# Kernel tuning notes

Hardware: AMD Instinct MI355X
Metric: run time of the kernel (lower is better)

The kernel has to match this reference:

```python
import jax, jax.numpy as jnp
import numpy as np

N, C_DEC, H, W = 16, 512, 32, 32
C_ENC, S, FEATS_IN, N_HEAD = 768, 77, 512, 8
EPS = 1e-5


def setup_inputs() -> dict:
    key = jax.random.key(0)
    ks = jax.random.split(key, 12)
    inp = {
        "input": jax.random.normal(ks[0], (N, C_DEC, H, W), jnp.float32),
        "cond": jax.random.normal(ks[1], (N, FEATS_IN), jnp.float32),
        "enc_hidden": jax.random.normal(ks[2], (N, S, C_ENC), jnp.float32),
        "enc_padding_mask": jax.random.randint(ks[3], (N, S), 0, 2).astype(jnp.float32),
        # AdaGN linear: feats_in -> 2*c_dec (scales, shifts)
        "adagn_w": jax.random.normal(ks[4], (2 * C_DEC, FEATS_IN), jnp.float32) * 0.02,
        "adagn_b": jnp.zeros((2 * C_DEC,), jnp.float32),
        # LayerNorm(c_enc) affine
        "ln_w": jnp.ones((C_ENC,), jnp.float32),
        "ln_b": jnp.zeros((C_ENC,), jnp.float32),
        # 1x1 conv q projection (treated as channel matmul)
        "q_w": jax.random.normal(ks[5], (C_DEC, C_DEC), jnp.float32) * 0.02,
        "q_b": jnp.zeros((C_DEC,), jnp.float32),
        # kv linear: c_enc -> 2*c_dec
        "kv_w": jax.random.normal(ks[6], (2 * C_DEC, C_ENC), jnp.float32) * 0.02,
        "kv_b": jnp.zeros((2 * C_DEC,), jnp.float32),
        # 1x1 conv out projection
        "out_w": jax.random.normal(ks[7], (C_DEC, C_DEC), jnp.float32) * 0.02,
        "out_b": jnp.zeros((C_DEC,), jnp.float32),
    }
    return inp


def reference(input, cond, enc_hidden, enc_padding_mask,
              adagn_w, adagn_b, ln_w, ln_b,
              q_w, q_b, kv_w, kv_b, out_w, out_b):
    n, c, h, w = input.shape
    d = c // N_HEAD

    # --- AdaGN: GroupNorm(1, c, affine=False) then cond-dependent scale/shift ---
    mu = jnp.mean(input, axis=(1, 2, 3), keepdims=True)
    var = jnp.var(input, axis=(1, 2, 3), keepdims=True)
    normed = (input - mu) * jax.lax.rsqrt(var + EPS)
    ss = cond @ adagn_w.T + adagn_b                      # [n, 2c]
    scales, shifts = ss[:, :c], ss[:, c:]
    x = shifts[:, :, None, None] + normed * (scales[:, :, None, None] + 1.0)

    # --- q projection (1x1 conv == per-pixel channel matmul) ---
    q = jnp.einsum('nchw,oc->nohw', x, q_w) + q_b[None, :, None, None]
    q = q.reshape(n, N_HEAD, d, h * w).transpose(0, 1, 3, 2)   # [n, head, hw, d]

    # --- encoder LayerNorm + kv projection ---
    mu_e = jnp.mean(enc_hidden, axis=-1, keepdims=True)
    var_e = jnp.var(enc_hidden, axis=-1, keepdims=True)
    e = (enc_hidden - mu_e) * jax.lax.rsqrt(var_e + EPS) * ln_w + ln_b
    kv = e @ kv_w.T + kv_b                               # [n, S, 2c]
    s = kv.shape[1]
    kv = kv.reshape(n, s, 2 * N_HEAD, d).transpose(0, 2, 1, 3)  # [n, 2*head, S, d]
    k, v = kv[:, :N_HEAD], kv[:, N_HEAD:]

    # --- scaled dot-product attention with additive padding mask ---
    scale = d ** (-0.25)
    att = jnp.einsum('nhqd,nhkd->nhqk', q * scale, k * scale)
    att = att - enc_padding_mask[:, None, None, :] * 10000.0
    att = jax.nn.softmax(att, axis=-1)
    y = jnp.einsum('nhqk,nhkd->nhqd', att, v)            # [n, head, hw, d]
    y = y.transpose(0, 1, 3, 2).reshape(n, c, h, w)

    out = jnp.einsum('nchw,oc->nohw', y, out_w) + out_b[None, :, None, None]
    return input + out
```

## Files before the change

kernel.cpp:

```cpp
#include <hip/hip_runtime.h>
#include <math.h>

typedef unsigned short u16;
typedef __bf16 bf16x8 __attribute__((ext_vector_type(8)));
typedef float f32x4 __attribute__((ext_vector_type(4)));

#define AS1 __attribute__((address_space(1)))
#define AS3 __attribute__((address_space(3)))

#define N_    16
#define C_    512
#define HW_   1024
#define CE_   768
#define S_    77
#define NH_   8
#define D_    64
#define FEATS_ 512
#define EPS_  1e-5f
#define TOK_  (N_ * S_)

#define WS_PSTAT 0
#define WS_QBIAS 1024
#define WSU_BYTE 131072
#define U_QW  0
#define U_OW  262144
#define U_KVW 524288
#define U_EB  1310720
#define U_KVB 2256896
#define U_YT  3518464
#define U_XT  11907072

__device__ __forceinline__ u16 f2bf(float f) {
    unsigned u = __float_as_uint(f);
    return (u16)((u + 0x7FFFu + ((u >> 16) & 1u)) >> 16);
}

__device__ __forceinline__ void gemm_mainloop(const u16* __restrict__ A, int lda, int arow0,
                                              const u16* __restrict__ B, int ldb, int brow0, int brmax,
                                              int K, f32x4 (&acc)[4][4], u16* As, u16* Bs) {
    int tid = threadIdx.x;
    int lane = tid & 63;
    int wm = ((tid >> 6) >> 1) * 64, wn = ((tid >> 6) & 1) * 64;
    int srow = tid >> 3;
    int sw = (tid & 7) ^ (srow & 7);
    int ldsoff = tid * 8;
    for (int kt = 0; kt < K; kt += 64) {
        __syncthreads();
#pragma unroll
        for (int i = 0; i < 4; i++) {
            int ar = arow0 + i * 32 + srow;
            const u16* ga = A + (size_t)ar * lda + kt + sw * 8;
            __builtin_amdgcn_global_load_lds((AS1 void*)ga, (AS3 void*)(As + i * 2048 + ldsoff), 16, 0, 0);
            int br = brow0 + i * 32 + srow; if (br > brmax) br = brmax;
            const u16* gb = B + (size_t)br * ldb + kt + sw * 8;
            __builtin_amdgcn_global_load_lds((AS1 void*)gb, (AS3 void*)(Bs + i * 2048 + ldsoff), 16, 0, 0);
        }
        __syncthreads();
#pragma unroll
        for (int kk = 0; kk < 2; kk++) {
            bf16x8 af[4], bfv[4];
            int ks = kk * 4 + (lane >> 4);
#pragma unroll
            for (int mi = 0; mi < 4; mi++) {
                int r = wm + mi * 16 + (lane & 15);
                af[mi] = *(const bf16x8*)(As + r * 64 + (ks ^ (r & 7)) * 8);
            }
#pragma unroll
            for (int ni = 0; ni < 4; ni++) {
                int r = wn + ni * 16 + (lane & 15);
                bfv[ni] = *(const bf16x8*)(Bs + r * 64 + (ks ^ (r & 7)) * 8);
            }
#pragma unroll
            for (int mi = 0; mi < 4; mi++)
#pragma unroll
                for (int ni = 0; ni < 4; ni++)
                    acc[mi][ni] = __builtin_amdgcn_mfma_f32_16x16x32_bf16(af[mi], bfv[ni], acc[mi][ni], 0, 0, 0);
        }
    }
}

__global__ __launch_bounds__(256) void mega1_kernel(const float* __restrict__ inp,
                                                    float* __restrict__ pstats,
                                                    const float* __restrict__ qw,
                                                    const float* __restrict__ ow,
                                                    const float* __restrict__ kvw,
                                                    u16* __restrict__ uq,
                                                    u16* __restrict__ uo,
                                                    u16* __restrict__ ukv,
                                                    const float* __restrict__ enc,
                                                    const float* __restrict__ lnw,
                                                    const float* __restrict__ lnb,
                                                    u16* __restrict__ eb,
                                                    const float* __restrict__ cond,
                                                    const float* __restrict__ agw,
                                                    const float* __restrict__ agb,
                                                    float* __restrict__ ssf) {
    __shared__ __align__(16) float smem[16384];
    int bid = blockIdx.x;
    int tid = threadIdx.x;
    if (bid < 256) {
        int n = bid >> 4, slice = bid & 15;
        const float* base = inp + (size_t)n * C_ * HW_ + slice * (C_ * HW_ / 16);
        float s = 0.f, s2 = 0.f;
        const float4* b4 = (const float4*)base;
        for (int i = tid; i < (C_ * HW_ / 16) / 4; i += 256) {
            float4 v = b4[i];
            s  += v.x + v.y + v.z + v.w;
            s2 += v.x * v.x + v.y * v.y + v.z * v.z + v.w * v.w;
        }
        for (int off = 32; off; off >>= 1) {
            s  += __shfl_down(s, off);
            s2 += __shfl_down(s2, off);
        }
        int wid = tid >> 6, lane = tid & 63;
        if (lane == 0) { smem[wid] = s; smem[4 + wid] = s2; }
        __syncthreads();
        if (tid == 0) {
            pstats[bid * 2]     = smem[0] + smem[1] + smem[2] + smem[3];
            pstats[bid * 2 + 1] = smem[4] + smem[5] + smem[6] + smem[7];
        }
    } else if (bid < 1536) {
        int i = (bid - 256) * 256 + tid;
        const float* s; u16* d; int j;
        if (i < 65536)       { s = qw;  d = uq;  j = i; }
        else if (i < 131072) { s = ow;  d = uo;  j = i - 65536; }
        else                 { s = kvw; d = ukv; j = i - 131072; }
        float4 v = ((const float4*)s)[j];
        ushort4 w;
        w.x = f2bf(v.x); w.y = f2bf(v.y); w.z = f2bf(v.z); w.w = f2bf(v.w);
        ((ushort4*)(d))[j] = w;
    } else if (bid < 2768) {
        int tok = bid - 1536;
        const float* row = enc + (size_t)tok * CE_;
        int t = tid;
        float v0 = row[t], v1 = row[t + 256], v2 = row[t + 512];
        float sum = v0 + v1 + v2;
        float sq  = v0 * v0 + v1 * v1 + v2 * v2;
        for (int off = 32; off; off >>= 1) {
            sum += __shfl_down(sum, off);
            sq  += __shfl_down(sq, off);
        }
        int wid = t >> 6, lane = t & 63;
        if (lane == 0) { smem[wid] = sum; smem[4 + wid] = sq; }
        __syncthreads();
        float tot = smem[0] + smem[1] + smem[2] + smem[3];
        float tsq = smem[4] + smem[5] + smem[6] + smem[7];
        float mu  = tot / CE_;
        float var = tsq / CE_ - mu * mu;
        float rstd = rsqrtf(var + EPS_);
        u16* o = eb + (size_t)tok * CE_;
        o[t]       = f2bf((v0 - mu) * rstd * lnw[t] + lnb[t]);
        o[t + 256] = f2bf((v1 - mu) * rstd * lnw[t + 256] + lnb[t + 256]);
        o[t + 512] = f2bf((v2 - mu) * rstd * lnw[t + 512] + lnb[t + 512]);
    } else {
        float (*wz)[512] = (float(*)[512])smem;
        float (*cz)[512] = (float(*)[512])(smem + 8192);
        int r0 = (bid - 2768) * 16;
        for (int i = tid; i < 2048; i += 256) {
            int row = i >> 7, f4 = i & 127;
            *(float4*)&cz[row][f4 * 4] = ((const float4*)(cond + (size_t)row * 512))[f4];
            *(float4*)&wz[row][f4 * 4] = ((const float4*)(agw + (size_t)(r0 + row) * 512))[f4];
        }
        __syncthreads();
        int n = tid >> 4, r = tid & 15;
        float acc = agb[r0 + r];
        for (int i = 0; i < 128; i++) {
            int j = (r + i) & 127;
            float4 c4 = *(const float4*)&cz[n][j * 4];
            float4 w4 = *(const float4*)&wz[r][j * 4];
            acc += c4.x * w4.x + c4.y * w4.y + c4.z * w4.z + c4.w * w4.w;
        }
        ssf[(size_t)n * 1024 + r0 + r] = acc;
    }
}

__global__ __launch_bounds__(256) void mega2_kernel(const float* __restrict__ inp,
                                                    const float* __restrict__ ssf,
                                                    const float* __restrict__ pstats,
                                                    u16* __restrict__ xT,
                                                    const float* __restrict__ qw,
                                                    const float* __restrict__ qb,
                                                    float* __restrict__ qbias,
                                                    const u16* __restrict__ kvwb,
                                                    const u16* __restrict__ eb,
                                                    const float* __restrict__ kvbias,
                                                    u16* __restrict__ kvo) {
    __shared__ __align__(16) float smem[16384];
    __shared__ float muS[16], rsS[16];
    int bid = blockIdx.x;
    int tid = threadIdx.x;
    float cnt = (float)(C_ * HW_);
    if (bid < 2048) {
        int n = bid >> 7, rem = bid & 127;
        int c0 = (rem >> 4) * 64, h0 = (rem & 15) * 64;
        float s = 0.f, s2 = 0.f;
        for (int k = 0; k < 16; k++) {
            s  += pstats[(n * 16 + k) * 2];
            s2 += pstats[(n * 16 + k) * 2 + 1];
        }
        float mu = s / cnt;
        float rstd = rsqrtf(s2 / cnt - mu * mu + EPS_);
        float (*t)[65] = (float(*)[65])smem;
        int rr = tid >> 4, cc = (tid & 15) * 4;
#pragma unroll
        for (int i = 0; i < 4; i++) {
            int cl = rr + i * 16;
            int c = c0 + cl;
            float a = rstd * (ssf[(size_t)n * 1024 + c] + 1.f);
            float4 v = *(const float4*)(inp + ((size_t)n * C_ + c) * HW_ + h0 + cc);
            t[cl][cc + 0] = v.x * a; t[cl][cc + 1] = v.y * a;
            t[cl][cc + 2] = v.z * a; t[cl][cc + 3] = v.w * a;
        }
        __syncthreads();
#pragma unroll
        for (int i = 0; i < 4; i++) {
            int hl = rr + i * 16;
            ushort4 w;
            w.x = f2bf(t[cc + 0][hl]); w.y = f2bf(t[cc + 1][hl]);
            w.z = f2bf(t[cc + 2][hl]); w.w = f2bf(t[cc + 3][hl]);
            *(ushort4*)(xT + ((size_t)n * HW_ + h0 + hl) * C_ + c0 + cc) = w;
        }
    } else if (bid < 2080) {
        float (*wz)[512] = (float(*)[512])smem;
        float (*cz)[512] = (float(*)[512])(smem + 8192);
        int r0 = (bid - 2048) * 16;
        if (tid < 16) {
            float s = 0.f, s2 = 0.f;
            for (int k = 0; k < 16; k++) {
                s  += pstats[(tid * 16 + k) * 2];
                s2 += pstats[(tid * 16 + k) * 2 + 1];
            }
            float mu = s / cnt;
            muS[tid] = mu;
            rsS[tid] = rsqrtf(s2 / cnt - mu * mu + EPS_);
        }
        __syncthreads();
        for (int i = tid; i < 2048; i += 256) {
            int row = i >> 7, f4 = i & 127;
            float4 sc4 = ((const float4*)(ssf + (size_t)row * 1024))[f4];
            float4 sh4 = ((const float4*)(ssf + (size_t)row * 1024 + 512))[f4];
            float mu = muS[row], rs = rsS[row];
            float4 b;
            b.x = sh4.x - mu * (rs * (sc4.x + 1.f));
            b.y = sh4.y - mu * (rs * (sc4.y + 1.f));
            b.z = sh4.z - mu * (rs * (sc4.z + 1.f));
            b.w = sh4.w - mu * (rs * (sc4.w + 1.f));
            *(float4*)&cz[row][f4 * 4] = b;
            *(float4*)&wz[row][f4 * 4] = ((const float4*)(qw + (size_t)(r0 + row) * 512))[f4];
        }
        __syncthreads();
        int n = tid >> 4, r = tid & 15;
        float acc = qb[r0 + r];
        for (int i = 0; i < 128; i++) {
            int j = (r + i) & 127;
            float4 c4 = *(const float4*)&cz[n][j * 4];
            float4 w4 = *(const float4*)&wz[r][j * 4];
            acc += c4.x * w4.x + c4.y * w4.y + c4.z * w4.z + c4.w * w4.w;
        }
        qbias[(size_t)n * 512 + r0 + r] = acc;
    } else {
        u16* As = (u16*)smem;
        u16* Bs = (u16*)smem + 8192;
        int t = bid - 2080;
        int brow0 = (t % 10) * 128, arow0 = (t / 10) * 128;
        f32x4 acc[4][4];
#pragma unroll
        for (int mi = 0; mi < 4; mi++)
#pragma unroll
            for (int ni = 0; ni < 4; ni++) acc[mi][ni] = 0.f;
        gemm_mainloop(kvwb, CE_, arow0, eb, CE_, brow0, TOK_ - 1, CE_, acc, As, Bs);
        int lane = tid & 63, wid = tid >> 6;
        int wm = (wid >> 1) * 64, wn = (wid & 1) * 64;
        int g = lane >> 4, l15 = lane & 15;
#pragma unroll
        for (int mi = 0; mi < 4; mi++) {
            int row = arow0 + wm + mi * 16 + (g << 2);
            float4 b4 = *(const float4*)(kvbias + row);
#pragma unroll
            for (int ni = 0; ni < 4; ni++) {
                int col = brow0 + wn + ni * 16 + l15;
                if (col < TOK_) {
                    f32x4 v = acc[mi][ni];
                    ushort4 wv;
                    wv.x = f2bf(v[0] + b4.x); wv.y = f2bf(v[1] + b4.y);
                    wv.z = f2bf(v[2] + b4.z); wv.w = f2bf(v[3] + b4.w);
                    *(ushort4*)(kvo + (size_t)col * 1024 + row) = wv;
                }
            }
        }
    }
}

__global__ __launch_bounds__(256) void mega3_kernel(const u16* __restrict__ qwb,
                                                    const u16* __restrict__ xT,
                                                    const float* __restrict__ qbias,
                                                    const u16* __restrict__ kvo,
                                                    const float* __restrict__ mask,
                                                    u16* __restrict__ yt) {
    __shared__ __align__(16) u16 pool[16384];
    __shared__ __align__(16) u16 Ks[80 * 64];
    __shared__ __align__(16) u16 VT[64 * 104];
    __shared__ __align__(16) u16 Ps[64 * 104];
    __shared__ float msk[80];
    u16* As = pool;
    u16* Bs = pool + 8192;
    int bid = blockIdx.x;
    int tid = threadIdx.x;
    int lane = tid & 63, w = tid >> 6;
    int g = lane >> 4, l15 = lane & 15;
    int wm = (w >> 1) * 64, wn = (w & 1) * 64;
    f32x4 acc[4][4];
#pragma unroll
    for (int mi = 0; mi < 4; mi++)
#pragma unroll
        for (int ni = 0; ni < 4; ni++) acc[mi][ni] = 0.f;

    int n = bid >> 5, r = bid & 31;
    int brow0 = (r & 7) * 128, arow0 = (r >> 3) * 128;
    gemm_mainloop(qwb, C_, arow0, xT + (size_t)n * HW_ * C_, C_, brow0, HW_ - 1, C_, acc, As, Bs);
    __syncthreads();

    const float* qbn = qbias + n * C_;
#pragma unroll
    for (int mi = 0; mi < 4; mi++) {
        int o_loc = wm + mi * 16 + g * 4;
        float4 b4 = *(const float4*)(qbn + arow0 + o_loc);
#pragma unroll
        for (int ni = 0; ni < 4; ni++) {
            int hw_loc = wn + ni * 16 + l15;
            f32x4 v = acc[mi][ni];
            ushort4 wv;
            wv.x = f2bf(v[0] + b4.x); wv.y = f2bf(v[1] + b4.y);
            wv.z = f2bf(v[2] + b4.z); wv.w = f2bf(v[3] + b4.w);
            int dd = o_loc & 63, hsel = o_loc >> 6;
            int col = hsel * 64 + (((dd >> 3) ^ (hw_loc & 7)) << 3) + (dd & 7);
            *(ushort4*)&pool[hw_loc * 128 + col] = wv;
        }
    }
    for (int i = tid; i < 512; i += 256) {
        int rr = i >> 3, cp = i & 7;
        *(unsigned*)&Ps[rr * 104 + 80 + cp * 2] = 0u;
    }
    if (tid < 80) msk[tid] = (tid < S_) ? mask[n * S_ + tid] * 10000.f : 0.f;
    __syncthreads();

    int h_base = arow0 >> 6;
    for (int hl = 0; hl < 2; hl++) {
        int h = h_base + hl;
        if (hl) __syncthreads();
        const u16* kbase = kvo + (size_t)(n * S_) * 1024 + h * 64;
#pragma unroll
        for (int pass = 0; pass < 3; pass++) {
            int idx = pass * 256 + tid;
            if (idx < 640) {
                int row = idx >> 3, slot = idx & 7;
                int srow = row < S_ ? row : S_ - 1;
                int sw = slot ^ (row & 7);
                __builtin_amdgcn_global_load_lds((AS1 void*)(kbase + (size_t)srow * 1024 + sw * 8),
                                                 (AS3 void*)(Ks + idx * 8), 16, 0, 0);
            }
        }
        {
            int d = tid & 63, sg = tid >> 6;
            const u16* vbase = kvo + (size_t)(n * S_) * 1024 + 512 + h * 64 + d;
            for (int s = sg; s < 104; s += 4) {
                u16 v = (s < S_) ? vbase[(size_t)s * 1024] : (u16)0;
                VT[d * 104 + s] = v;
            }
        }
        __syncthreads();

        for (int qhalf = 0; qhalf < 2; qhalf++) {
            int qrl = qhalf * 64 + w * 16 + l15;
            bf16x8 qf[2];
#pragma unroll
            for (int kk = 0; kk < 2; kk++) {
                int s8 = kk * 4 + g;
                qf[kk] = *(const bf16x8*)(pool + qrl * 128 + hl * 64 + ((s8 ^ (qrl & 7)) << 3));
            }
            f32x4 sc[5];
#pragma unroll
            for (int kb = 0; kb < 5; kb++) {
                sc[kb] = 0.f;
#pragma unroll
                for (int kk = 0; kk < 2; kk++) {
                    int rr = kb * 16 + l15;
                    int s8 = kk * 4 + g;
                    bf16x8 kf = *(const bf16x8*)(Ks + rr * 64 + ((s8 ^ (rr & 7)) << 3));
                    sc[kb] = __builtin_amdgcn_mfma_f32_16x16x32_bf16(kf, qf[kk], sc[kb], 0, 0, 0);
                }
            }
            float sv[5][4];
            float mx = -3e38f;
#pragma unroll
            for (int kb = 0; kb < 5; kb++)
#pragma unroll
                for (int j = 0; j < 4; j++) {
                    int key = kb * 16 + g * 4 + j;
                    float s = sc[kb][j] * 0.125f - msk[key];
                    sv[kb][j] = s;
                    if (key < S_) mx = fmaxf(mx, s);
                }
            mx = fmaxf(mx, __shfl_xor(mx, 16));
            mx = fmaxf(mx, __shfl_xor(mx, 32));
            float sum = 0.f;
            float p[5][4];
#pragma unroll
            for (int kb = 0; kb < 5; kb++)
#pragma unroll
                for (int j = 0; j < 4; j++) {
                    int key = kb * 16 + g * 4 + j;
                    float pv = (key < S_) ? __expf(sv[kb][j] - mx) : 0.f;
                    p[kb][j] = pv;
                    sum += pv;
                }
            sum += __shfl_xor(sum, 16);
            sum += __shfl_xor(sum, 32);
            float inv = 1.f / sum;
            int prow = w * 16 + l15;
#pragma unroll
            for (int kb = 0; kb < 5; kb++) {
                unsigned lo = (unsigned)f2bf(p[kb][0] * inv) | ((unsigned)f2bf(p[kb][1] * inv) << 16);
                unsigned hi = (unsigned)f2bf(p[kb][2] * inv) | ((unsigned)f2bf(p[kb][3] * inv) << 16);
                int col = kb * 16 + g * 4;
                *(uint2*)&Ps[prow * 104 + col] = make_uint2(lo, hi);
            }
            f32x4 ya[4];
#pragma unroll
            for (int mf = 0; mf < 4; mf++) ya[mf] = 0.f;
#pragma unroll
            for (int kk = 0; kk < 3; kk++) {
                int s8 = kk * 4 + g;
                bf16x8 pf = *(const bf16x8*)(Ps + prow * 104 + s8 * 8);
#pragma unroll
                for (int mf = 0; mf < 4; mf++) {
                    bf16x8 vf = *(const bf16x8*)(VT + (mf * 16 + l15) * 104 + s8 * 8);
                    ya[mf] = __builtin_amdgcn_mfma_f32_16x16x32_bf16(vf, pf, ya[mf], 0, 0, 0);
                }
            }
            u16* yrow = yt + ((size_t)(n * HW_ + brow0 + qrl)) * C_ + h * 64;
#pragma unroll
            for (int mf = 0; mf < 4; mf++) {
                int d0 = mf * 16 + g * 4;
                ushort4 o;
                o.x = f2bf(ya[mf][0]); o.y = f2bf(ya[mf][1]);
                o.z = f2bf(ya[mf][2]); o.w = f2bf(ya[mf][3]);
                *(ushort4*)(yrow + d0) = o;
            }
        }
    }
}

__global__ __launch_bounds__(256) void gemm_out_mfma(const u16* __restrict__ owb,
                                                     const u16* __restrict__ yT,
                                                     const float* __restrict__ ob,
                                                     const float* __restrict__ inp,
                                                     float* __restrict__ outp) {
    __shared__ __align__(16) u16 As[128 * 64];
    __shared__ __align__(16) u16 Bs[128 * 64];
    int n = blockIdx.z;
    int arow0 = blockIdx.y * 128, brow0 = blockIdx.x * 128;
    f32x4 acc[4][4];
#pragma unroll
    for (int mi = 0; mi < 4; mi++)
#pragma unroll
        for (int ni = 0; ni < 4; ni++) acc[mi][ni] = 0.f;
    gemm_mainloop(owb, C_, arow0, yT + (size_t)n * HW_ * C_, C_, brow0, HW_ - 1, C_, acc, As, Bs);
    int lane = threadIdx.x & 63, wid = threadIdx.x >> 6;
    int wm = (wid >> 1) * 64, wn = (wid & 1) * 64;
    float* Co = outp + (size_t)n * C_ * HW_;
    const float* In = inp + (size_t)n * C_ * HW_;
#pragma unroll
    for (int mi = 0; mi < 4; mi++) {
        int row = arow0 + wm + mi * 16 + ((lane >> 4) << 2);
        float4 b4 = *(const float4*)(ob + row);
#pragma unroll
        for (int ni = 0; ni < 4; ni++) {
            int col = brow0 + wn + ni * 16 + (lane & 15);
            f32x4 v = acc[mi][ni];
            size_t i0 = (size_t)row * HW_ + col;
            Co[i0]            = v[0] + b4.x + In[i0];
            Co[i0 + HW_]      = v[1] + b4.y + In[i0 + HW_];
            Co[i0 + 2 * HW_]  = v[2] + b4.z + In[i0 + 2 * HW_];
            Co[i0 + 3 * HW_]  = v[3] + b4.w + In[i0 + 3 * HW_];
        }
    }
}

extern "C" void kernel_launch(void* const* d_in, const int* in_sizes, int n_in,
                              void* d_out, int out_size, void* d_ws, size_t ws_size,
                              hipStream_t stream) {
    const float* inp  = (const float*)d_in[0];
    const float* cond = (const float*)d_in[1];
    const float* enc  = (const float*)d_in[2];
    const float* mask = (const float*)d_in[3];
    const float* agw  = (const float*)d_in[4];
    const float* agb  = (const float*)d_in[5];
    const float* lnw  = (const float*)d_in[6];
    const float* lnb  = (const float*)d_in[7];
    const float* qw   = (const float*)d_in[8];
    const float* qb   = (const float*)d_in[9];
    const float* kvw  = (const float*)d_in[10];
    const float* kvb  = (const float*)d_in[11];
    const float* ow   = (const float*)d_in[12];
    const float* ob   = (const float*)d_in[13];
    float* ws  = (float*)d_ws;
    float* out = (float*)d_out;
    u16* wsu = (u16*)((char*)d_ws + WSU_BYTE);
    float* ssf = (float*)(wsu + U_YT);

    mega1_kernel<<<dim3(2832), 256, 0, stream>>>(inp, ws + WS_PSTAT,
                                                 qw, ow, kvw, wsu + U_QW, wsu + U_OW, wsu + U_KVW,
                                                 enc, lnw, lnb, wsu + U_EB,
                                                 cond, agw, agb, ssf);
    mega2_kernel<<<dim3(2160), 256, 0, stream>>>(inp, ssf, ws + WS_PSTAT,
                                                 wsu + U_XT, qw, qb, ws + WS_QBIAS,
                                                 wsu + U_KVW, wsu + U_EB, kvb, wsu + U_KVB);
    mega3_kernel<<<dim3(512), 256, 0, stream>>>(wsu + U_QW, wsu + U_XT, ws + WS_QBIAS,
                                                wsu + U_KVB, mask, wsu + U_YT);

    gemm_out_mfma<<<dim3(HW_ / 128, C_ / 128, N_), 256, 0, stream>>>(
        wsu + U_OW, wsu + U_YT, ob, inp, out);
}
```

Before: 100.6 us.

## Fuse four phase kernels into one cooperative persistent kernel with grid syncs

Replaces the four separate kernel launches with a single cooperative kernel of 512 persistent blocks. Each block walks its share of work units per phase, with grid.sync between phases, and falls back to four ordinary launches if the cooperative launch fails. Phase work is reordered: the AdaGN matvec moves first, the KV GEMM comes first in phase 2, and the matvecs now read weights from global memory instead of staging them in shared memory. Shared memory is unified into one buffer of about 60KB so two blocks fit per CU. The aim is to remove launch gaps and tail effects between kernels, at the cost of grid-sync overhead and fewer resident blocks for the bandwidth-bound phases.

Measured after the change: 276.6 us. 2.75x slower.

```diff
diff --git a/kernel.cpp b/kernel.cpp
--- a/kernel.cpp
+++ b/kernel.cpp
@@ -1,5 +1,8 @@
 #include <hip/hip_runtime.h>
+#include <hip/hip_cooperative_groups.h>
 #include <math.h>
+
+namespace cg = cooperative_groups;
 
 typedef unsigned short u16;
 typedef __bf16 bf16x8 __attribute__((ext_vector_type(8)));
@@ -15,9 +18,9 @@
 #define S_    77
 #define NH_   8
 #define D_    64
-#define FEATS_ 512
 #define EPS_  1e-5f
 #define TOK_  (N_ * S_)
+#define NBLK  512
 
 #define WS_PSTAT 0
 #define WS_QBIAS 1024
@@ -30,10 +33,23 @@
 #define U_YT  3518464
 #define U_XT  11907072
 
+#define L_SIZE 29888
+#define LO_BS   8192
+#define LO_VT   16384
+#define LO_PS   23040
+#define LO_MSK  29696
+
 __device__ __forceinline__ u16 f2bf(float f) {
     unsigned u = __float_as_uint(f);
     return (u16)((u + 0x7FFFu + ((u >> 16) & 1u)) >> 16);
 }
+
+struct Params {
+    const float *inp, *cond, *enc, *mask, *agw, *agb, *lnw, *lnb, *qw, *qb, *kvw, *kvb, *ow, *ob;
+    float *pstats, *qbias, *ssf;
+    u16 *uq, *uo, *ukv, *eb, *kvo, *xT, *yt;
+    float *outp;
+};
 
 __device__ __forceinline__ void gemm_mainloop(const u16* __restrict__ A, int lda, int arow0,
                                               const u16* __restrict__ B, int ldb, int brow0, int brmax,
@@ -79,28 +95,31 @@
     }
 }
 
-__global__ __launch_bounds__(256) void mega1_kernel(const float* __restrict__ inp,
-                                                    float* __restrict__ pstats,
-                                                    const float* __restrict__ qw,
-                                                    const float* __restrict__ ow,
-                                                    const float* __restrict__ kvw,
-                                                    u16* __restrict__ uq,
-                                                    u16* __restrict__ uo,
-                                                    u16* __restrict__ ukv,
-                                                    const float* __restrict__ enc,
-                                                    const float* __restrict__ lnw,
-                                                    const float* __restrict__ lnb,
-                                                    u16* __restrict__ eb,
-                                                    const float* __restrict__ cond,
-                                                    const float* __restrict__ agw,
-                                                    const float* __restrict__ agb,
-                                                    float* __restrict__ ssf) {
-    __shared__ __align__(16) float smem[16384];
-    int bid = blockIdx.x;
+__device__ __forceinline__ void phase1_unit(const Params& p, int u, u16* L) {
+    float* smem = (float*)L;
     int tid = threadIdx.x;
-    if (bid < 256) {
-        int n = bid >> 4, slice = bid & 15;
-        const float* base = inp + (size_t)n * C_ * HW_ + slice * (C_ * HW_ / 16);
+    if (u < 64) {
+        float (*cz)[512] = (float(*)[512])smem;
+        int r0 = u * 16;
+        for (int i = tid; i < 2048; i += 256) {
+            int row = i >> 7, f4 = i & 127;
+            *(float4*)&cz[row][f4 * 4] = ((const float4*)(p.cond + (size_t)row * 512))[f4];
+        }
+        __syncthreads();
+        int n = tid >> 4, r = tid & 15;
+        float acc = p.agb[r0 + r];
+        const float4* wrow = (const float4*)(p.agw + (size_t)(r0 + r) * 512);
+        for (int i = 0; i < 128; i++) {
+            int j = (r + i) & 127;
+            float4 c4 = *(const float4*)&cz[n][j * 4];
+            float4 w4 = wrow[j];
+            acc += c4.x * w4.x + c4.y * w4.y + c4.z * w4.z + c4.w * w4.w;
+        }
+        p.ssf[(size_t)n * 1024 + r0 + r] = acc;
+    } else if (u < 320) {
+        int b = u - 64;
+        int n = b >> 4, slice = b & 15;
+        const float* base = p.inp + (size_t)n * C_ * HW_ + slice * (C_ * HW_ / 16);
         float s = 0.f, s2 = 0.f;
         const float4* b4 = (const float4*)base;
         for (int i = tid; i < (C_ * HW_ / 16) / 4; i += 256) {
@@ -116,22 +135,22 @@
         if (lane == 0) { smem[wid] = s; smem[4 + wid] = s2; }
         __syncthreads();
         if (tid == 0) {
-            pstats[bid * 2]     = smem[0] + smem[1] + smem[2] + smem[3];
-            pstats[bid * 2 + 1] = smem[4] + smem[5] + smem[6] + smem[7];
-        }
-    } else if (bid < 1536) {
-        int i = (bid - 256) * 256 + tid;
+            p.pstats[b * 2]     = smem[0] + smem[1] + smem[2] + smem[3];
+            p.pstats[b * 2 + 1] = smem[4] + smem[5] + smem[6] + smem[7];
+        }
+    } else if (u < 1600) {
+        int i = (u - 320) * 256 + tid;
         const float* s; u16* d; int j;
-        if (i < 65536)       { s = qw;  d = uq;  j = i; }
-        else if (i < 131072) { s = ow;  d = uo;  j = i - 65536; }
-        else                 { s = kvw; d = ukv; j = i - 131072; }
+        if (i < 65536)       { s = p.qw;  d = p.uq;  j = i; }
+        else if (i < 131072) { s = p.ow;  d = p.uo;  j = i - 65536; }
+        else                 { s = p.kvw; d = p.ukv; j = i - 131072; }
         float4 v = ((const float4*)s)[j];
         ushort4 w;
         w.x = f2bf(v.x); w.y = f2bf(v.y); w.z = f2bf(v.z); w.w = f2bf(v.w);
         ((ushort4*)(d))[j] = w;
-    } else if (bid < 2768) {
-        int tok = bid - 1536;
-        const float* row = enc + (size_t)tok * CE_;
+    } else {
+        int tok = u - 1600;
+        const float* row = p.enc + (size_t)tok * CE_;
         int t = tid;
         float v0 = row[t], v1 = row[t + 256], v2 = row[t + 512];
         float sum = v0 + v1 + v2;
@@ -146,89 +165,56 @@
         float tot = smem[0] + smem[1] + smem[2] + smem[3];
         float tsq = smem[4] + smem[5] + smem[6] + smem[7];
         float mu  = tot / CE_;
-        float var = tsq / CE_ - mu * mu;
-        float rstd = rsqrtf(var + EPS_);
-        u16* o = eb + (size_t)tok * CE_;
-        o[t]       = f2bf((v0 - mu) * rstd * lnw[t] + lnb[t]);
-        o[t + 256] = f2bf((v1 - mu) * rstd * lnw[t + 256] + lnb[t + 256]);
-        o[t + 512] = f2bf((v2 - mu) * rstd * lnw[t + 512] + lnb[t + 512]);
-    } else {
-        float (*wz)[512] = (float(*)[512])smem;
-        float (*cz)[512] = (float(*)[512])(smem + 8192);
-        int r0 = (bid - 2768) * 16;
-        for (int i = tid; i < 2048; i += 256) {
-            int row = i >> 7, f4 = i & 127;
-            *(float4*)&cz[row][f4 * 4] = ((const float4*)(cond + (size_t)row * 512))[f4];
-            *(float4*)&wz[row][f4 * 4] = ((const float4*)(agw + (size_t)(r0 + row) * 512))[f4];
-        }
-        __syncthreads();
-        int n = tid >> 4, r = tid & 15;
-        float acc = agb[r0 + r];
-        for (int i = 0; i < 128; i++) {
-            int j = (r + i) & 127;
-            float4 c4 = *(const float4*)&cz[n][j * 4];
-            float4 w4 = *(const float4*)&wz[r][j * 4];
-            acc += c4.x * w4.x + c4.y * w4.y + c4.z * w4.z + c4.w * w4.w;
-        }
-        ssf[(size_t)n * 1024 + r0 + r] = acc;
-    }
-}
-
-__global__ __launch_bounds__(256) void mega2_kernel(const float* __restrict__ inp,
-                                                    const float* __restrict__ ssf,
-                                                    const float* __restrict__ pstats,
-                                                    u16* __restrict__ xT,
-                                                    const float* __restrict__ qw,
-                                                    const float* __restrict__ qb,
-                                                    float* __restrict__ qbias,
-                                                    const u16* __restrict__ kvwb,
-                                                    const u16* __restrict__ eb,
-                                                    const float* __restrict__ kvbias,
-                                                    u16* __restrict__ kvo) {
-    __shared__ __align__(16) float smem[16384];
-    __shared__ float muS[16], rsS[16];
-    int bid = blockIdx.x;
+        float rstd = rsqrtf(tsq / CE_ - mu * mu + EPS_);
+        u16* o = p.eb + (size_t)tok * CE_;
+        o[t]       = f2bf((v0 - mu) * rstd * p.lnw[t] + p.lnb[t]);
+        o[t + 256] = f2bf((v1 - mu) * rstd * p.lnw[t + 256] + p.lnb[t + 256]);
+        o[t + 512] = f2bf((v2 - mu) * rstd * p.lnw[t + 512] + p.lnb[t + 512]);
+    }
+}
+
+__device__ __forceinline__ void phase2_unit(const Params& p, int u, u16* L) {
+    float* smem = (float*)L;
     int tid = threadIdx.x;
     float cnt = (float)(C_ * HW_);
-    if (bid < 2048) {
-        int n = bid >> 7, rem = bid & 127;
-        int c0 = (rem >> 4) * 64, h0 = (rem & 15) * 64;
-        float s = 0.f, s2 = 0.f;
-        for (int k = 0; k < 16; k++) {
-            s  += pstats[(n * 16 + k) * 2];
-            s2 += pstats[(n * 16 + k) * 2 + 1];
-        }
-        float mu = s / cnt;
-        float rstd = rsqrtf(s2 / cnt - mu * mu + EPS_);
-        float (*t)[65] = (float(*)[65])smem;
-        int rr = tid >> 4, cc = (tid & 15) * 4;
-#pragma unroll
-        for (int i = 0; i < 4; i++) {
-            int cl = rr + i * 16;
-            int c = c0 + cl;
-            float a = rstd * (ssf[(size_t)n * 1024 + c] + 1.f);
-            float4 v = *(const float4*)(inp + ((size_t)n * C_ + c) * HW_ + h0 + cc);
-            t[cl][cc + 0] = v.x * a; t[cl][cc + 1] = v.y * a;
-            t[cl][cc + 2] = v.z * a; t[cl][cc + 3] = v.w * a;
-        }
-        __syncthreads();
-#pragma unroll
-        for (int i = 0; i < 4; i++) {
-            int hl = rr + i * 16;
-            ushort4 w;
-            w.x = f2bf(t[cc + 0][hl]); w.y = f2bf(t[cc + 1][hl]);
-            w.z = f2bf(t[cc + 2][hl]); w.w = f2bf(t[cc + 3][hl]);
-            *(ushort4*)(xT + ((size_t)n * HW_ + h0 + hl) * C_ + c0 + cc) = w;
-        }
-    } else if (bid < 2080) {
-        float (*wz)[512] = (float(*)[512])smem;
-        float (*cz)[512] = (float(*)[512])(smem + 8192);
-        int r0 = (bid - 2048) * 16;
+    if (u < 80) {
+        u16* As = L; u16* Bs = L + LO_BS;
+        int brow0 = (u % 10) * 128, arow0 = (u / 10) * 128;
+        f32x4 acc[4][4];
+#pragma unroll
+        for (int mi = 0; mi < 4; mi++)
+#pragma unroll
+            for (int ni = 0; ni < 4; ni++) acc[mi][ni] = 0.f;
+        gemm_mainloop(p.ukv, CE_, arow0, p.eb, CE_, brow0, TOK_ - 1, CE_, acc, As, Bs);
+        int lane = tid & 63, wid = tid >> 6;
+        int wm = (wid >> 1) * 64, wn = (wid & 1) * 64;
+        int g = lane >> 4, l15 = lane & 15;
+#pragma unroll
+        for (int mi = 0; mi < 4; mi++) {
+            int row = arow0 + wm + mi * 16 + (g << 2);
+            float4 b4 = *(const float4*)(p.kvb + row);
+#pragma unroll
+            for (int ni = 0; ni < 4; ni++) {
+                int col = brow0 + wn + ni * 16 + l15;
+                if (col < TOK_) {
+                    f32x4 v = acc[mi][ni];
+                    ushort4 wv;
+                    wv.x = f2bf(v[0] + b4.x); wv.y = f2bf(v[1] + b4.y);
+                    wv.z = f2bf(v[2] + b4.z); wv.w = f2bf(v[3] + b4.w);
+                    *(ushort4*)(p.kvo + (size_t)col * 1024 + row) = wv;
+                }
+            }
+        }
+    } else if (u < 112) {
+        float (*cz)[512] = (float(*)[512])smem;
+        float* muS = (float*)(L + LO_MSK);
+        float* rsS = muS + 16;
+        int r0 = (u - 80) * 16;
         if (tid < 16) {
             float s = 0.f, s2 = 0.f;
             for (int k = 0; k < 16; k++) {
-                s  += pstats[(tid * 16 + k) * 2];
-                s2 += pstats[(tid * 16 + k) * 2 + 1];
+                s  += p.pstats[(tid * 16 + k) * 2];
+                s2 += p.pstats[(tid * 16 + k) * 2 + 1];
             }
             float mu = s / cnt;
             muS[tid] = mu;
@@ -237,8 +223,8 @@
         __syncthreads();
         for (int i = tid; i < 2048; i += 256) {
             int row = i >> 7, f4 = i & 127;
-            float4 sc4 = ((const float4*)(ssf + (size_t)row * 1024))[f4];
-            float4 sh4 = ((const float4*)(ssf + (size_t)row * 1024 + 512))[f4];
+            float4 sc4 = ((const float4*)(p.ssf + (size_t)row * 1024))[f4];
+            float4 sh4 = ((const float4*)(p.ssf + (size_t)row * 1024 + 512))[f4];
             float mu = muS[row], rs = rsS[row];
             float4 b;
             b.x = sh4.x - mu * (rs * (sc4.x + 1.f));
@@ -246,65 +232,60 @@
             b.z = sh4.z - mu * (rs * (sc4.z + 1.f));
             b.w = sh4.w - mu * (rs * (sc4.w + 1.f));
             *(float4*)&cz[row][f4 * 4] = b;
-            *(float4*)&wz[row][f4 * 4] = ((const float4*)(qw + (size_t)(r0 + row) * 512))[f4];
         }
         __syncthreads();
         int n = tid >> 4, r = tid & 15;
-        float acc = qb[r0 + r];
+        float acc = p.qb[r0 + r];
+        const float4* wrow = (const float4*)(p.qw + (size_t)(r0 + r) * 512);
         for (int i = 0; i < 128; i++) {
             int j = (r + i) & 127;
             float4 c4 = *(const float4*)&cz[n][j * 4];
-            float4 w4 = *(const float4*)&wz[r][j * 4];
+            float4 w4 = wrow[j];
             acc += c4.x * w4.x + c4.y * w4.y + c4.z * w4.z + c4.w * w4.w;
         }
-        qbias[(size_t)n * 512 + r0 + r] = acc;
+        p.qbias[(size_t)n * 512 + r0 + r] = acc;
     } else {
-        u16* As = (u16*)smem;
-        u16* Bs = (u16*)smem + 8192;
-        int t = bid - 2080;
-        int brow0 = (t % 10) * 128, arow0 = (t / 10) * 128;
-        f32x4 acc[4][4];
-#pragma unroll
-        for (int mi = 0; mi < 4; mi++)
-#pragma unroll
-            for (int ni = 0; ni < 4; ni++) acc[mi][ni] = 0.f;
-        gemm_mainloop(kvwb, CE_, arow0, eb, CE_, brow0, TOK_ - 1, CE_, acc, As, Bs);
-        int lane = tid & 63, wid = tid >> 6;
-        int wm = (wid >> 1) * 64, wn = (wid & 1) * 64;
-        int g = lane >> 4, l15 = lane & 15;
-#pragma unroll
-        for (int mi = 0; mi < 4; mi++) {
-            int row = arow0 + wm + mi * 16 + (g << 2);
-            float4 b4 = *(const float4*)(kvbias + row);
-#pragma unroll
-            for (int ni = 0; ni < 4; ni++) {
-                int col = brow0 + wn + ni * 16 + l15;
-                if (col < TOK_) {
-                    f32x4 v = acc[mi][ni];
-                    ushort4 wv;
-                    wv.x = f2bf(v[0] + b4.x); wv.y = f2bf(v[1] + b4.y);
-                    wv.z = f2bf(v[2] + b4.z); wv.w = f2bf(v[3] + b4.w);
-                    *(ushort4*)(kvo + (size_t)col * 1024 + row) = wv;
-                }
-            }
-        }
-    }
-}
-
-__global__ __launch_bounds__(256) void mega3_kernel(const u16* __restrict__ qwb,
-                                                    const u16* __restrict__ xT,
-                                                    const float* __restrict__ qbias,
-                                                    const u16* __restrict__ kvo,
-                                                    const float* __restrict__ mask,
-                                                    u16* __restrict__ yt) {
-    __shared__ __align__(16) u16 pool[16384];
-    __shared__ __align__(16) u16 Ks[80 * 64];
-    __shared__ __align__(16) u16 VT[64 * 104];
-    __shared__ __align__(16) u16 Ps[64 * 104];
-    __shared__ float msk[80];
-    u16* As = pool;
-    u16* Bs = pool + 8192;
-    int bid = blockIdx.x;
+        int bid2 = u - 112;
+        int n = bid2 >> 7, rem = bid2 & 127;
+        int c0 = (rem >> 4) * 64, h0 = (rem & 15) * 64;
+        float s = 0.f, s2 = 0.f;
+        for (int k = 0; k < 16; k++) {
+            s  += p.pstats[(n * 16 + k) * 2];
+            s2 += p.pstats[(n * 16 + k) * 2 + 1];
+        }
+        float mu = s / cnt;
+        float rstd = rsqrtf(s2 / cnt - mu * mu + EPS_);
+        float (*t)[65] = (float(*)[65])smem;
+        int rr = tid >> 4, cc = (tid & 15) * 4;
+#pragma unroll
+        for (int i = 0; i < 4; i++) {
+            int cl = rr + i * 16;
+            int c = c0 + cl;
+            float a = rstd * (p.ssf[(size_t)n * 1024 + c] + 1.f);
+            float4 v = *(const float4*)(p.inp + ((size_t)n * C_ + c) * HW_ + h0 + cc);
+            t[cl][cc + 0] = v.x * a; t[cl][cc + 1] = v.y * a;
+            t[cl][cc + 2] = v.z * a; t[cl][cc + 3] = v.w * a;
+        }
+        __syncthreads();
+#pragma unroll
+        for (int i = 0; i < 4; i++) {
+            int hl = rr + i * 16;
+            ushort4 w;
+            w.x = f2bf(t[cc + 0][hl]); w.y = f2bf(t[cc + 1][hl]);
+            w.z = f2bf(t[cc + 2][hl]); w.w = f2bf(t[cc + 3][hl]);
+            *(ushort4*)(p.xT + ((size_t)n * HW_ + h0 + hl) * C_ + c0 + cc) = w;
+        }
+    }
+}
+
+__device__ __forceinline__ void phase3_unit(const Params& p, int bid, u16* L) {
+    u16* As = L;
+    u16* Bs = L + LO_BS;
+    u16* Qs2 = L;
+    u16* Ks  = L + LO_BS;
+    u16* VT  = L + LO_VT;
+    u16* Ps  = L + LO_PS;
+    float* msk = (float*)(L + LO_MSK);
     int tid = threadIdx.x;
     int lane = tid & 63, w = tid >> 6;
     int g = lane >> 4, l15 = lane & 15;
@@ -317,52 +298,55 @@
 
     int n = bid >> 5, r = bid & 31;
     int brow0 = (r & 7) * 128, arow0 = (r >> 3) * 128;
-    gemm_mainloop(qwb, C_, arow0, xT + (size_t)n * HW_ * C_, C_, brow0, HW_ - 1, C_, acc, As, Bs);
+    int h_base = arow0 >> 6;
+    gemm_mainloop(p.uq, C_, arow0, p.xT + (size_t)n * HW_ * C_, C_, brow0, HW_ - 1, C_, acc, As, Bs);
     __syncthreads();
 
-    const float* qbn = qbias + n * C_;
-#pragma unroll
-    for (int mi = 0; mi < 4; mi++) {
-        int o_loc = wm + mi * 16 + g * 4;
-        float4 b4 = *(const float4*)(qbn + arow0 + o_loc);
-#pragma unroll
-        for (int ni = 0; ni < 4; ni++) {
-            int hw_loc = wn + ni * 16 + l15;
-            f32x4 v = acc[mi][ni];
-            ushort4 wv;
-            wv.x = f2bf(v[0] + b4.x); wv.y = f2bf(v[1] + b4.y);
-            wv.z = f2bf(v[2] + b4.z); wv.w = f2bf(v[3] + b4.w);
-            int dd = o_loc & 63, hsel = o_loc >> 6;
-            int col = hsel * 64 + (((dd >> 3) ^ (hw_loc & 7)) << 3) + (dd & 7);
-            *(ushort4*)&pool[hw_loc * 128 + col] = wv;
-        }
-    }
     for (int i = tid; i < 512; i += 256) {
         int rr = i >> 3, cp = i & 7;
         *(unsigned*)&Ps[rr * 104 + 80 + cp * 2] = 0u;
     }
-    if (tid < 80) msk[tid] = (tid < S_) ? mask[n * S_ + tid] * 10000.f : 0.f;
-    __syncthreads();
-
-    int h_base = arow0 >> 6;
+    if (tid < 80) msk[tid] = (tid < S_) ? p.mask[n * S_ + tid] * 10000.f : 0.f;
+
+    const float* qbn = p.qbias + n * C_ + arow0;
     for (int hl = 0; hl < 2; hl++) {
         int h = h_base + hl;
         if (hl) __syncthreads();
-        const u16* kbase = kvo + (size_t)(n * S_) * 1024 + h * 64;
-#pragma unroll
-        for (int pass = 0; pass < 3; pass++) {
-            int idx = pass * 256 + tid;
-            if (idx < 640) {
-                int row = idx >> 3, slot = idx & 7;
-                int srow = row < S_ ? row : S_ - 1;
-                int sw = slot ^ (row & 7);
-                __builtin_amdgcn_global_load_lds((AS1 void*)(kbase + (size_t)srow * 1024 + sw * 8),
-                                                 (AS3 void*)(Ks + idx * 8), 16, 0, 0);
+        {
+            const u16* kbase = p.kvo + (size_t)(n * S_) * 1024 + h * 64;
+#pragma unroll
+            for (int pass = 0; pass < 3; pass++) {
+                int idx = pass * 256 + tid;
+                if (idx < 640) {
+                    int row = idx >> 3, slot = idx & 7;
+                    int srow = row < S_ ? row : S_ - 1;
+                    int sw = slot ^ (row & 7);
+                    __builtin_amdgcn_global_load_lds((AS1 void*)(kbase + (size_t)srow * 1024 + sw * 8),
+                                                     (AS3 void*)(Ks + idx * 8), 16, 0, 0);
+                }
+            }
+        }
+        if ((wm >> 6) == hl) {
+#pragma unroll
+            for (int mi = 0; mi < 4; mi++) {
+                int o_loc = wm + mi * 16 + g * 4;
+                float4 b4 = *(const float4*)(qbn + o_loc);
+                int dd = o_loc & 63;
+#pragma unroll
+                for (int ni = 0; ni < 4; ni++) {
+                    int hw_loc = wn + ni * 16 + l15;
+                    f32x4 v = acc[mi][ni];
+                    ushort4 wv;
+                    wv.x = f2bf(v[0] + b4.x); wv.y = f2bf(v[1] + b4.y);
+                    wv.z = f2bf(v[2] + b4.z); wv.w = f2bf(v[3] + b4.w);
+                    int col = (((dd >> 3) ^ (hw_loc & 7)) << 3) + (dd & 7);
+                    *(ushort4*)&Qs2[hw_loc * 64 + col] = wv;
+                }
             }
         }
         {
             int d = tid & 63, sg = tid >> 6;
-            const u16* vbase = kvo + (size_t)(n * S_) * 1024 + 512 + h * 64 + d;
+            const u16* vbase = p.kvo + (size_t)(n * S_) * 1024 + 512 + h * 64 + d;
             for (int s = sg; s < 104; s += 4) {
                 u16 v = (s < S_) ? vbase[(size_t)s * 1024] : (u16)0;
                 VT[d * 104 + s] = v;
@@ -376,7 +360,7 @@
 #pragma unroll
             for (int kk = 0; kk < 2; kk++) {
                 int s8 = kk * 4 + g;
-                qf[kk] = *(const bf16x8*)(pool + qrl * 128 + hl * 64 + ((s8 ^ (qrl & 7)) << 3));
+                qf[kk] = *(const bf16x8*)(Qs2 + qrl * 64 + ((s8 ^ (qrl & 7)) << 3));
             }
             f32x4 sc[5];
 #pragma unroll
@@ -404,14 +388,14 @@
             mx = fmaxf(mx, __shfl_xor(mx, 16));
             mx = fmaxf(mx, __shfl_xor(mx, 32));
             float sum = 0.f;
-            float p[5][4];
+            float pw[5][4];
 #pragma unroll
             for (int kb = 0; kb < 5; kb++)
 #pragma unroll
                 for (int j = 0; j < 4; j++) {
                     int key = kb * 16 + g * 4 + j;
                     float pv = (key < S_) ? __expf(sv[kb][j] - mx) : 0.f;
-                    p[kb][j] = pv;
+                    pw[kb][j] = pv;
                     sum += pv;
                 }
             sum += __shfl_xor(sum, 16);
@@ -420,8 +404,8 @@
             int prow = w * 16 + l15;
 #pragma unroll
             for (int kb = 0; kb < 5; kb++) {
-                unsigned lo = (unsigned)f2bf(p[kb][0] * inv) | ((unsigned)f2bf(p[kb][1] * inv) << 16);
-                unsigned hi = (unsigned)f2bf(p[kb][2] * inv) | ((unsigned)f2bf(p[kb][3] * inv) << 16);
+                unsigned lo = (unsigned)f2bf(pw[kb][0] * inv) | ((unsigned)f2bf(pw[kb][1] * inv) << 16);
+                unsigned hi = (unsigned)f2bf(pw[kb][2] * inv) | ((unsigned)f2bf(pw[kb][3] * inv) << 16);
                 int col = kb * 16 + g * 4;
                 *(uint2*)&Ps[prow * 104 + col] = make_uint2(lo, hi);
             }
@@ -438,7 +422,7 @@
                     ya[mf] = __builtin_amdgcn_mfma_f32_16x16x32_bf16(vf, pf, ya[mf], 0, 0, 0);
                 }
             }
-            u16* yrow = yt + ((size_t)(n * HW_ + brow0 + qrl)) * C_ + h * 64;
+            u16* yrow = p.yt + ((size_t)(n * HW_ + brow0 + qrl)) * C_ + h * 64;
 #pragma unroll
             for (int mf = 0; mf < 4; mf++) {
                 int d0 = mf * 16 + g * 4;
@@ -451,74 +435,109 @@
     }
 }
 
-__global__ __launch_bounds__(256) void gemm_out_mfma(const u16* __restrict__ owb,
-                                                     const u16* __restrict__ yT,
-                                                     const float* __restrict__ ob,
-                                                     const float* __restrict__ inp,
-                                                     float* __restrict__ outp) {
-    __shared__ __align__(16) u16 As[128 * 64];
-    __shared__ __align__(16) u16 Bs[128 * 64];
-    int n = blockIdx.z;
-    int arow0 = blockIdx.y * 128, brow0 = blockIdx.x * 128;
+__device__ __forceinline__ void phase4_unit(const Params& p, int bid, u16* L) {
+    u16* As = L; u16* Bs = L + LO_BS;
+    int tid = threadIdx.x;
+    int n = bid >> 5, r = bid & 31;
+    int arow0 = (r >> 3) * 128, brow0 = (r & 7) * 128;
     f32x4 acc[4][4];
 #pragma unroll
     for (int mi = 0; mi < 4; mi++)
 #pragma unroll
         for (int ni = 0; ni < 4; ni++) acc[mi][ni] = 0.f;
-    gemm_mainloop(owb, C_, arow0, yT + (size_t)n * HW_ * C_, C_, brow0, HW_ - 1, C_, acc, As, Bs);
-    int lane = threadIdx.x & 63, wid = threadIdx.x >> 6;
+    gemm_mainloop(p.uo, C_, arow0, p.yt + (size_t)n * HW_ * C_, C_, brow0, HW_ - 1, C_, acc, As, Bs);
+    int lane = tid & 63, wid = tid >> 6;
     int wm = (wid >> 1) * 64, wn = (wid & 1) * 64;
-    float* Co = outp + (size_t)n * C_ * HW_;
-    const float* In = inp + (size_t)n * C_ * HW_;
+    float* Co = p.outp + (size_t)n * C_ * HW_;
+    const float* In = p.inp + (size_t)n * C_ * HW_;
 #pragma unroll
     for (int mi = 0; mi < 4; mi++) {
         int row = arow0 + wm + mi * 16 + ((lane >> 4) << 2);
-        float4 b4 = *(const float4*)(ob + row);
+        float4 b4 = *(const float4*)(p.ob + row);
 #pragma unroll
         for (int ni = 0; ni < 4; ni++) {
             int col = brow0 + wn + ni * 16 + (lane & 15);
             f32x4 v = acc[mi][ni];
             size_t i0 = (size_t)row * HW_ + col;
-            Co[i0]            = v[0] + b4.x + In[i0];
-            Co[i0 + HW_]      = v[1] + b4.y + In[i0 + HW_];
-            Co[i0 + 2 * HW_]  = v[2] + b4.z + In[i0 + 2 * HW_];
-            Co[i0 + 3 * HW_]  = v[3] + b4.w + In[i0 + 3 * HW_];
-        }
-    }
+            Co[i0]           = v[0] + b4.x + In[i0];
+            Co[i0 + HW_]     = v[1] + b4.y + In[i0 + HW_];
+            Co[i0 + 2 * HW_] = v[2] + b4.z + In[i0 + 2 * HW_];
+            Co[i0 + 3 * HW_] = v[3] + b4.w + In[i0 + 3 * HW_];
+        }
+    }
+}
+
+__global__ __launch_bounds__(256, 2) void fused_coop(Params p) {
+    __shared__ __align__(16) u16 L[L_SIZE];
+    cg::grid_group grid = cg::this_grid();
+    int bid = blockIdx.x;
+    for (int u = bid; u < 2832; u += NBLK) { __syncthreads(); phase1_unit(p, u, L); }
+    grid.sync();
+    for (int u = bid; u < 2160; u += NBLK) { __syncthreads(); phase2_unit(p, u, L); }
+    grid.sync();
+    phase3_unit(p, bid, L);
+    grid.sync();
+    phase4_unit(p, bid, L);
+}
+
+__global__ __launch_bounds__(256) void p1_kernel(Params p) {
+    __shared__ __align__(16) u16 L[L_SIZE];
+    phase1_unit(p, blockIdx.x, L);
+}
+__global__ __launch_bounds__(256) void p2_kernel(Params p) {
+    __shared__ __align__(16) u16 L[L_SIZE];
+    phase2_unit(p, blockIdx.x, L);
+}
+__global__ __launch_bounds__(256) void p3_kernel(Params p) {
+    __shared__ __align__(16) u16 L[L_SIZE];
+    phase3_unit(p, blockIdx.x, L);
+}
+__global__ __launch_bounds__(256) void p4_kernel(Params p) {
+    __shared__ __align__(16) u16 L[L_SIZE];
+    phase4_unit(p, blockIdx.x, L);
 }
 
 extern "C" void kernel_launch(void* const* d_in, const int* in_sizes, int n_in,
                               void* d_out, int out_size, void* d_ws, size_t ws_size,
                               hipStream_t stream) {
-    const float* inp  = (const float*)d_in[0];
-    const float* cond = (const float*)d_in[1];
-    const float* enc  = (const float*)d_in[2];
-    const float* mask = (const float*)d_in[3];
-    const float* agw  = (const float*)d_in[4];
-    const float* agb  = (const float*)d_in[5];
-    const float* lnw  = (const float*)d_in[6];
-    const float* lnb  = (const float*)d_in[7];
-    const float* qw   = (const float*)d_in[8];
-    const float* qb   = (const float*)d_in[9];
-    const float* kvw  = (const float*)d_in[10];
-    const float* kvb  = (const float*)d_in[11];
-    const float* ow   = (const float*)d_in[12];
-    const float* ob   = (const float*)d_in[13];
     float* ws  = (float*)d_ws;
-    float* out = (float*)d_out;
     u16* wsu = (u16*)((char*)d_ws + WSU_BYTE);
-    float* ssf = (float*)(wsu + U_YT);
-
-    mega1_kernel<<<dim3(2832), 256, 0, stream>>>(inp, ws + WS_PSTAT,
-                                                 qw, ow, kvw, wsu + U_QW, wsu + U_OW, wsu + U_KVW,
-                                                 enc, lnw, lnb, wsu + U_EB,
-                                                 cond, agw, agb, ssf);
-    mega2_kernel<<<dim3(2160), 256, 0, stream>>>(inp, ssf, ws + WS_PSTAT,
-                                                 wsu + U_XT, qw, qb, ws + WS_QBIAS,
-                                                 wsu + U_KVW, wsu + U_EB, kvb, wsu + U_KVB);
-    mega3_kernel<<<dim3(512), 256, 0, stream>>>(wsu + U_QW, wsu + U_XT, ws + WS_QBIAS,
-                                                wsu + U_KVB, mask, wsu + U_YT);
-
-    gemm_out_mfma<<<dim3(HW_ / 128, C_ / 128, N_), 256, 0, stream>>>(
-        wsu + U_OW, wsu + U_YT, ob, inp, out);
-}
+
+    Params p;
+    p.inp  = (const float*)d_in[0];
+    p.cond = (const float*)d_in[1];
+    p.enc  = (const float*)d_in[2];
+    p.mask = (const float*)d_in[3];
+    p.agw  = (const float*)d_in[4];
+    p.agb  = (const float*)d_in[5];
+    p.lnw  = (const float*)d_in[6];
+    p.lnb  = (const float*)d_in[7];
+    p.qw   = (const float*)d_in[8];
+    p.qb   = (const float*)d_in[9];
+    p.kvw  = (const float*)d_in[10];
+    p.kvb  = (const float*)d_in[11];
+    p.ow   = (const float*)d_in[12];
+    p.ob   = (const float*)d_in[13];
+    p.pstats = ws + WS_PSTAT;
+    p.qbias  = ws + WS_QBIAS;
+    p.ssf    = (float*)(wsu + U_YT);
+    p.uq  = wsu + U_QW;
+    p.uo  = wsu + U_OW;
+    p.ukv = wsu + U_KVW;
+    p.eb  = wsu + U_EB;
+    p.kvo = wsu + U_KVB;
+    p.xT  = wsu + U_XT;
+    p.yt  = wsu + U_YT;
+    p.outp = (float*)d_out;
+
+    void* kargs[] = { &p };
+    hipError_t rc = hipLaunchCooperativeKernel(reinterpret_cast<void*>(fused_coop),
+                                               dim3(NBLK), dim3(256), kargs, 0, stream);
+    if (rc != hipSuccess) {
+        (void)hipGetLastError();
+        p1_kernel<<<dim3(2832), 256, 0, stream>>>(p);
+        p2_kernel<<<dim3(2160), 256, 0, stream>>>(p);
+        p3_kernel<<<dim3(512), 256, 0, stream>>>(p);
+        p4_kernel<<<dim3(512), 256, 0, stream>>>(p);
+    }
+}
```
